# Kernel optimization log

Measured on AMD Instinct MI355X. Metric: run time of the kernel, lower is better.

The kernel has to match this reference:

```python
import jax, jax.numpy as jnp
import numpy as np

B, NH, M, XD = 8192, 128, 4096, 1024
ALPHA_1, SIGMA_1 = 100.0, 0.02
MAX_ITER = 30  # FastBarrierProjectionNoUpper(max_iter=30)


def cayley(W):
    """Cayley orthogonalization of a (possibly rectangular) matrix (out, in)."""
    cout, cin = W.shape
    if cout < cin:
        return cayley(W.T).T
    U, V = W[:cin], W[cin:]                 # U: (cin,cin), V: (cout-cin,cin)
    I = jnp.eye(cin, dtype=W.dtype)
    A = U - U.T + V.T @ V                   # skew + Gram
    iIpA = jnp.linalg.inv(I + A)
    return jnp.concatenate([iIpA @ (I - A), -2.0 * V @ iIpA], axis=0)


def cayley_linear(x, W, b, alpha):
    Q = cayley(alpha * W / jnp.linalg.norm(W))
    return x @ Q.T + b


def project_no_upper(lower, f_tilde):
    """Projection of f_tilde onto {f : sum(f)=0, f >= lower} per row.
    f*(lam) = max(f_tilde - lam, lower); Newton on g(lam)=sum f*(lam)=0,
    iterated a fixed MAX_ITER times (matches the 30-iter barrier solver)."""
    lam0 = jnp.mean(f_tilde, axis=-1, keepdims=True)

    def step(lam, _):
        f = jnp.maximum(f_tilde - lam, lower)
        g = jnp.sum(f, axis=-1, keepdims=True)
        active = jnp.sum((f_tilde - lam > lower).astype(f.dtype), axis=-1, keepdims=True)
        dg = -jnp.maximum(active, 1.0)      # g'(lam), safeguarded
        return lam - g / dg, None

    lam, _ = jax.lax.scan(step, lam0, None, length=MAX_ITER)
    return jnp.maximum(f_tilde - lam, lower)


def setup_inputs() -> dict:
    key = jax.random.key(0)
    ks = jax.random.split(key, 8)
    h = jax.random.uniform(ks[0], (B, NH), dtype=jnp.float32)
    h = h / jnp.sum(h, axis=-1, keepdims=True)      # state lives on the simplex
    x = jax.random.normal(ks[1], (B, XD), dtype=jnp.float32)

    def mk_w(k, shape):
        return jax.random.normal(k, shape, dtype=jnp.float32) * 0.05

    W_hm = mk_w(ks[2], (M, NH))
    W_mm = mk_w(ks[3], (M, M))
    W_mh = mk_w(ks[4], (NH, M))
    W_ux = mk_w(ks[5], (M, XD))
    b_hm = jnp.zeros((M,), jnp.float32)
    b_mm = jnp.zeros((M,), jnp.float32)
    b_mh = jnp.zeros((NH,), jnp.float32)
    b_ux = jnp.zeros((M,), jnp.float32)
    # CayleyLinear alpha initialized to ||W||_F (so alpha*W/||W|| == W at init)
    a_hm = jnp.linalg.norm(W_hm)
    a_mm = jnp.linalg.norm(W_mm)
    a_mh = jnp.linalg.norm(W_mh)
    a_ux = jnp.linalg.norm(W_ux)
    return {"h": h, "x": x,
            "W_hm": W_hm, "b_hm": b_hm, "a_hm": a_hm,
            "W_mm": W_mm, "b_mm": b_mm, "a_mm": a_mm,
            "W_mh": W_mh, "b_mh": b_mh, "a_mh": a_mh,
            "W_ux": W_ux, "b_ux": b_ux, "a_ux": a_ux}


def reference(h, x, W_hm, b_hm, a_hm, W_mm, b_mm, a_mm,
              W_mh, b_mh, a_mh, W_ux, b_ux, a_ux):
    # _h_dot_raw (dropout identity in eval mode)
    z = cayley_linear(h, W_hm, b_hm, a_hm) + cayley_linear(x, W_ux, b_ux, a_ux)
    z = jax.nn.relu(z)
    z = jax.nn.relu(cayley_linear(z, W_mm, b_mm, a_mm))
    f_tilde = cayley_linear(z, W_mh, b_mh, a_mh)   # [B, NH]
    # barrier lower bound keeping h >= 0 forward-invariant
    lower = -ALPHA_1 * (jnp.exp(SIGMA_1 * h) - 1.0)
    return project_no_upper(lower, f_tilde)
```

## Files before the change

kernel.cpp:

```cpp
#include <hip/hip_runtime.h>
#include <math.h>

#define ALPHA_1 100.0f
#define SIGMA_1 0.02f

typedef unsigned short bf16_t;
typedef short  bf16x8  __attribute__((ext_vector_type(8)));
typedef float  floatx4 __attribute__((ext_vector_type(4)));

typedef __attribute__((address_space(1))) void glb_void;
typedef __attribute__((address_space(3))) void lds_void;

__device__ __forceinline__ float bf2f(bf16_t u){ return __uint_as_float(((unsigned)u)<<16); }
__device__ __forceinline__ bf16_t f2bf(float f){
  unsigned u = __float_as_uint(f);
  u += 0x7FFFu + ((u>>16)&1u);
  return (bf16_t)(u>>16);
}

__device__ __forceinline__ void split4(float4 v, ushort4& h, ushort4& l){
  h.x=f2bf(v.x); h.y=f2bf(v.y); h.z=f2bf(v.z); h.w=f2bf(v.w);
  l.x=f2bf(v.x-bf2f(h.x)); l.y=f2bf(v.y-bf2f(h.y));
  l.z=f2bf(v.z-bf2f(h.z)); l.w=f2bf(v.w-bf2f(h.w));
}

__device__ __forceinline__ float4 load4f(const float* p){ return *(const float4*)p; }
__device__ __forceinline__ float loadS(const float* p){ return *p; }
__device__ __forceinline__ float loadS(const bf16_t* p){ return bf2f(*p); }
__device__ __forceinline__ void storeS(float* p, float v){ *p = v; }
__device__ __forceinline__ void storeS(bf16_t* p, float v){ *p = f2bf(v); }

__device__ __forceinline__ void async_copy16(void* lds, const void* g){
  __builtin_amdgcn_global_load_lds((glb_void*)g, (lds_void*)lds, 16, 0, 0);
}

template<typename TC, int RELU>
__global__ __launch_bounds__(256) void mfma_nt_kernel(
    int Mm, int Nn, int Kk,
    const bf16_t* __restrict__ A, int lda,
    const bf16_t* __restrict__ B, int ldb,
    TC* __restrict__ C, int ldc,
    const float* __restrict__ bias)
{
  __shared__ bf16_t As[128*64];
  __shared__ bf16_t Bs[128*64];
  const int tid  = threadIdx.x;
  const int lane = tid & 63, wv = tid >> 6;
  const int m0 = (int)(blockIdx.y << 7), n0 = (int)(blockIdx.x << 7);
  const int wm = (wv >> 1) << 6, wn = (wv & 1) << 6;
  const int rbase = wv << 5;

  floatx4 acc[4][4] = {};

  for (int kk = 0; kk < Kk; kk += 64){
    __syncthreads();
#pragma unroll
    for (int q=0;q<4;q++){
      int row = rbase + (q<<3) + (lane>>3);
      int cg  = (lane&7) ^ (row&7);
      async_copy16(&As[(size_t)(rbase+(q<<3))<<6],
                   A + (size_t)(m0+row)*lda + kk + (cg<<3));
      async_copy16(&Bs[(size_t)(rbase+(q<<3))<<6],
                   B + (size_t)(n0+row)*ldb + kk + (cg<<3));
    }
    __syncthreads();
#pragma unroll
    for (int ks=0; ks<2; ks++){
      bf16x8 af[4], bf[4];
      int quad = lane>>4, mr = lane&15;
      int c = quad + (ks<<2);
#pragma unroll
      for (int i=0;i<4;i++){
        int rowa = wm + i*16 + mr;
        af[i] = *(const bf16x8*)&As[(rowa<<6) + ((c ^ (rowa&7))<<3)];
        int rowb = wn + i*16 + mr;
        bf[i] = *(const bf16x8*)&Bs[(rowb<<6) + ((c ^ (rowb&7))<<3)];
      }
#pragma unroll
      for (int i=0;i<4;i++)
#pragma unroll
        for (int j=0;j<4;j++)
          acc[i][j] = __builtin_amdgcn_mfma_f32_16x16x32_bf16(af[i], bf[j], acc[i][j], 0,0,0);
    }
  }
#pragma unroll
  for (int i=0;i<4;i++){
#pragma unroll
    for (int j=0;j<4;j++){
      int rbase2 = m0 + wm + i*16 + (lane>>4)*4;
      int col    = n0 + wn + j*16 + (lane&15);
      float bv = bias ? bias[col] : 0.0f;
#pragma unroll
      for (int r=0;r<4;r++){
        float v = acc[i][j][r] + bv;
        if (RELU) v = fmaxf(v, 0.0f);
        storeS(&C[(size_t)(rbase2+r)*ldc + col], v);
      }
    }
  }
}

template<typename TC>
__global__ __launch_bounds__(256) void fgemm_nt_kernel(
    int Mm, int Nn, int Kk,
    const float* __restrict__ A, int lda,
    const float* __restrict__ Bt, int ldb,
    TC* __restrict__ C, int ldc,
    float alpha, const float* __restrict__ alpha_ptr, float beta, int skipk)
{
  __shared__ bf16_t Ah[128*64], Al[128*64], Bh[128*64], Bl[128*64];
  const int tid = threadIdx.x;
  const int lane = tid & 63, wv = tid >> 6;
  int by = blockIdx.y; if (by >= skipk) by++;
  const int m0 = by << 7, n0 = blockIdx.x << 7;
  const int wm = (wv >> 1) << 6, wn = (wv & 1) << 6;
  floatx4 acc[4][4] = {};

  for (int kk = 0; kk < Kk; kk += 64){
    float4 va[8], vb[8];
#pragma unroll
    for (int i=0;i<8;i++){
      int idx = (tid<<3) + i;
      int row = idx >> 4;
      int cg  = idx & 15;
      va[i] = load4f(A  + (size_t)(m0+row)*lda + kk + (cg<<2));
      vb[i] = load4f(Bt + (size_t)(n0+row)*ldb + kk + (cg<<2));
    }
    __syncthreads();
#pragma unroll
    for (int i=0;i<8;i++){
      int idx = (tid<<3) + i;
      int row = idx >> 4, cg = idx & 15;
      int off = (row<<6) + (((cg>>1) ^ (row&7))<<3) + ((cg&1)<<2);
      ushort4 hv, lv; split4(va[i], hv, lv);
      *(ushort4*)&Ah[off] = hv; *(ushort4*)&Al[off] = lv;
      ushort4 hw, lw; split4(vb[i], hw, lw);
      *(ushort4*)&Bh[off] = hw; *(ushort4*)&Bl[off] = lw;
    }
    __syncthreads();
#pragma unroll
    for (int ks=0; ks<2; ks++){
      int quad = lane>>4, mr = lane&15;
      int c = quad + (ks<<2);
      bf16x8 ah[4], al[4], bh[4], bl[4];
#pragma unroll
      for (int i=0;i<4;i++){
        int rowa = wm + i*16 + mr; int sa = (rowa<<6) + ((c ^ (rowa&7))<<3);
        ah[i] = *(const bf16x8*)&Ah[sa]; al[i] = *(const bf16x8*)&Al[sa];
        int rowb = wn + i*16 + mr; int sb = (rowb<<6) + ((c ^ (rowb&7))<<3);
        bh[i] = *(const bf16x8*)&Bh[sb]; bl[i] = *(const bf16x8*)&Bl[sb];
      }
#pragma unroll
      for (int i=0;i<4;i++)
#pragma unroll
        for (int j=0;j<4;j++){
          acc[i][j] = __builtin_amdgcn_mfma_f32_16x16x32_bf16(ah[i], bl[j], acc[i][j], 0,0,0);
          acc[i][j] = __builtin_amdgcn_mfma_f32_16x16x32_bf16(al[i], bh[j], acc[i][j], 0,0,0);
          acc[i][j] = __builtin_amdgcn_mfma_f32_16x16x32_bf16(ah[i], bh[j], acc[i][j], 0,0,0);
        }
    }
    __syncthreads();
  }
  float am = alpha;
  if (alpha_ptr) am *= *alpha_ptr;
#pragma unroll
  for (int i=0;i<4;i++){
#pragma unroll
    for (int j=0;j<4;j++){
      int rb = m0 + wm + i*16 + (lane>>4)*4;
      int col = n0 + wn + j*16 + (lane&15);
#pragma unroll
      for (int r=0;r<4;r++){
        size_t off = (size_t)(rb+r)*ldc + col;
        float v = am * acc[i][j][r];
        if (beta != 0.0f) v = fmaf(beta, loadS(&C[off]), v);
        storeS(&C[off], v);
      }
    }
  }
}

__global__ __launch_bounds__(1024) void invert128_kernel(
    const float* __restrict__ src, int ld,
    float* __restrict__ dst, float* __restrict__ dstT)
{
  __shared__ float brow[2][8*36];
  const int t = threadIdx.x;
  const int r = t>>3, sub = t&7;
  const int lane = t & 63;
  const int cb = (sub&3)<<5;
  const bool isA = sub < 4;
  float own[32];
  if (isA){
#pragma unroll
    for (int i=0;i<32;i++) own[i] = src[(size_t)r*ld + cb + i];
  } else {
#pragma unroll
    for (int i=0;i<32;i++) own[i] = (cb+i == r) ? 1.0f : 0.0f;
  }
  for (int pb=0; pb<4; pb++){
#pragma unroll
    for (int pi=0; pi<32; pi++){
      const int p = (pb<<5) + pi;
      float f = __shfl(own[pi], (lane & 56) | pb);
      float* bw = brow[p & 1];
      if (r == p){
        float ip = 1.0f / f;
#pragma unroll
        for (int i=0;i<32;i++) own[i] *= ip;
#pragma unroll
        for (int i=0;i<8;i++){
          float4 v;
          v.x = own[(i<<2)+0]; v.y = own[(i<<2)+1];
          v.z = own[(i<<2)+2]; v.w = own[(i<<2)+3];
          *(float4*)&bw[sub*36 + (i<<2)] = v;
        }
      }
      __syncthreads();
      if (r != p){
#pragma unroll
        for (int i=0;i<8;i++){
          float4 b = *(const float4*)&bw[sub*36 + (i<<2)];
          own[(i<<2)+0] = fmaf(-f, b.x, own[(i<<2)+0]);
          own[(i<<2)+1] = fmaf(-f, b.y, own[(i<<2)+1]);
          own[(i<<2)+2] = fmaf(-f, b.z, own[(i<<2)+2]);
          own[(i<<2)+3] = fmaf(-f, b.w, own[(i<<2)+3]);
        }
      }
    }
  }
  if (!isA){
#pragma unroll
    for (int i=0;i<32;i++){
      dst [(size_t)r*128 + cb + i] = own[i];
      dstT[(size_t)(cb+i)*128 + r] = own[i];
    }
  }
}


__device__ void tile_to_lds(
    const float* __restrict__ Min, int n, int k, int r, int c,
    const bf16_t* __restrict__ Gh, const bf16_t* __restrict__ Gl,
    const bf16_t* __restrict__ Th, const bf16_t* __restrict__ Tl,
    float* __restrict__ Dst, char* __restrict__ stage, int tid)
{
  if (c == k){
    const bf16_t* sh = Gh + ((size_t)r<<14);
    const bf16_t* sl = Gl + ((size_t)r<<14);
    for (int q=tid; q<4096; q+=1024){
      int rr=q>>5, c4=(q&31)<<2;
      ushort4 hv=*(const ushort4*)&sh[(rr<<7)+c4];
      ushort4 lv=*(const ushort4*)&sl[(rr<<7)+c4];
      Dst[rr*132+c4+0]=bf2f(hv.x)+bf2f(lv.x);
      Dst[rr*132+c4+1]=bf2f(hv.y)+bf2f(lv.y);
      Dst[rr*132+c4+2]=bf2f(hv.z)+bf2f(lv.z);
      Dst[rr*132+c4+3]=bf2f(hv.w)+bf2f(lv.w);
    }
    __syncthreads();
    return;
  }
  bf16_t* Ah=(bf16_t*)stage;           bf16_t* Al=(bf16_t*)(stage+16384);
  bf16_t* Bh=(bf16_t*)(stage+32768);   bf16_t* Bl=(bf16_t*)(stage+49152);
  const int lane = tid & 63, wv = tid >> 6;
  const int wm = (wv >> 2) << 5, wn = (wv & 3) << 5;
  const bf16_t* gh = Gh + ((size_t)r<<14);
  const bf16_t* gl = Gl + ((size_t)r<<14);
  const bf16_t* th = Th + ((size_t)c<<14);
  const bf16_t* tl = Tl + ((size_t)c<<14);
  floatx4 acc[2][2] = {};
#pragma unroll
  for (int kk = 0; kk < 128; kk += 64){
    __syncthreads();
#pragma unroll
    for (int s=0;s<2;s++){
      int idx = tid + (s<<10);
      int row = idx >> 4, cg = idx & 15;
      int off = (row<<6) + (((cg>>1) ^ (row&7))<<3) + ((cg&1)<<2);
      *(ushort4*)&Ah[off] = *(const ushort4*)&gh[(row<<7) + kk + (cg<<2)];
      *(ushort4*)&Al[off] = *(const ushort4*)&gl[(row<<7) + kk + (cg<<2)];
      *(ushort4*)&Bh[off] = *(const ushort4*)&th[(row<<7) + kk + (cg<<2)];
      *(ushort4*)&Bl[off] = *(const ushort4*)&tl[(row<<7) + kk + (cg<<2)];
    }
    __syncthreads();
#pragma unroll
    for (int ks=0; ks<2; ks++){
      int quad = lane>>4, mr = lane&15;
      int cc = quad + (ks<<2);
      bf16x8 ah[2], al[2], bh[2], bl[2];
#pragma unroll
      for (int i=0;i<2;i++){
        int rowa = wm + i*16 + mr; int sa = (rowa<<6) + ((cc ^ (rowa&7))<<3);
        ah[i] = *(const bf16x8*)&Ah[sa]; al[i] = *(const bf16x8*)&Al[sa];
        int rowb = wn + i*16 + mr; int sb = (rowb<<6) + ((cc ^ (rowb&7))<<3);
        bh[i] = *(const bf16x8*)&Bh[sb]; bl[i] = *(const bf16x8*)&Bl[sb];
      }
#pragma unroll
      for (int i=0;i<2;i++)
#pragma unroll
        for (int j=0;j<2;j++){
          acc[i][j] = __builtin_amdgcn_mfma_f32_16x16x32_bf16(ah[i], bl[j], acc[i][j], 0,0,0);
          acc[i][j] = __builtin_amdgcn_mfma_f32_16x16x32_bf16(al[i], bh[j], acc[i][j], 0,0,0);
          acc[i][j] = __builtin_amdgcn_mfma_f32_16x16x32_bf16(ah[i], bh[j], acc[i][j], 0,0,0);
        }
    }
  }
  const int addin = (r != k);
#pragma unroll
  for (int i=0;i<2;i++)
#pragma unroll
    for (int j=0;j<2;j++){
      int rb = wm + i*16 + ((lane>>4)<<2);
      int col = wn + j*16 + (lane&15);
#pragma unroll
      for (int r4=0;r4<4;r4++){
        float v = acc[i][j][r4];
        if (addin) v += Min[(size_t)((r<<7)+rb+r4)*n + (c<<7) + col];
        Dst[(rb+r4)*132 + col] = v;
      }
    }
  __syncthreads();
}

__device__ void prep1024(
    const float* __restrict__ Mc, int n, int k, int ib,
    bf16_t* __restrict__ Gh, bf16_t* __restrict__ Gl,
    bf16_t* __restrict__ Th, bf16_t* __restrict__ Tl,
    char* smraw, int t)
{
  float* browB = (float*)smraw;
  float* Pl    = (float*)(smraw + 2304);
  float* Ast   = (float*)(smraw + 69888);
  const int r = t>>3, sub = t&7;
  const int lane = t & 63;
  const int cb = (sub&3)<<5;
  const bool isA = sub < 4;
  const float* D = Mc + ((size_t)(k<<7))*n + (k<<7);
  float own[32];
  if (isA){
#pragma unroll
    for (int q=0;q<32;q++) own[q] = D[(size_t)r*n + cb + q];
  } else {
#pragma unroll
    for (int q=0;q<32;q++) own[q] = (cb+q == r) ? 1.0f : 0.0f;
  }
  for (int pb=0; pb<4; pb++){
#pragma unroll
    for (int pi=0; pi<32; pi++){
      const int p = (pb<<5) + pi;
      float f = __shfl(own[pi], (lane & 56) | pb);
      float* bw = browB + (p & 1)*288;
      if (r == p){
        float ip = 1.0f / f;
#pragma unroll
        for (int q=0;q<32;q++) own[q] *= ip;
#pragma unroll
        for (int q=0;q<8;q++){
          float4 v;
          v.x=own[(q<<2)+0]; v.y=own[(q<<2)+1]; v.z=own[(q<<2)+2]; v.w=own[(q<<2)+3];
          *(float4*)&bw[sub*36 + (q<<2)] = v;
        }
      }
      __syncthreads();
      if (r != p){
#pragma unroll
        for (int q=0;q<8;q++){
          float4 b = *(const float4*)&bw[sub*36 + (q<<2)];
          own[(q<<2)+0] = fmaf(-f, b.x, own[(q<<2)+0]);
          own[(q<<2)+1] = fmaf(-f, b.y, own[(q<<2)+1]);
          own[(q<<2)+2] = fmaf(-f, b.z, own[(q<<2)+2]);
          own[(q<<2)+3] = fmaf(-f, b.w, own[(q<<2)+3]);
        }
      }
    }
  }
  if (!isA){
#pragma unroll
    for (int q=0;q<8;q++){
      float4 v;
      v.x=own[(q<<2)+0]; v.y=own[(q<<2)+1]; v.z=own[(q<<2)+2]; v.w=own[(q<<2)+3];
      *(float4*)&Pl[r*132 + cb + (q<<2)] = v;
      if (ib == k){
        ushort4 hv, lv; split4(v, hv, lv);
        *(ushort4*)&Gh[((size_t)k<<14) + (r<<7) + cb + (q<<2)] = hv;
        *(ushort4*)&Gl[((size_t)k<<14) + (r<<7) + cb + (q<<2)] = lv;
      }
    }
  }
  __syncthreads();
  if (ib == k) return;

  const float* Ski = Mc + ((size_t)(k<<7))*n + (ib<<7);
#pragma unroll
  for (int q=0;q<4;q++){
    int f4 = (t<<2) + q;
    int rr = f4>>5, c4 = (f4&31)<<2;
    *(float4*)&Ast[rr*132 + c4] = *(const float4*)&Ski[(size_t)rr*n + c4];
  }
  __syncthreads();
#pragma unroll
  for (int q=0;q<4;q++){
    int f4 = (t<<2) + q;
    int cc = f4>>5, r4 = (f4&31)<<2;
    float4 v;
    v.x = Ast[(r4+0)*132 + cc]; v.y = Ast[(r4+1)*132 + cc];
    v.z = Ast[(r4+2)*132 + cc]; v.w = Ast[(r4+3)*132 + cc];
    ushort4 hv, lv; split4(v, hv, lv);
    *(ushort4*)&Th[((size_t)ib<<14) + (cc<<7) + r4] = hv;
    *(ushort4*)&Tl[((size_t)ib<<14) + (cc<<7) + r4] = lv;
  }
  __syncthreads();

  const float* Sik = Mc + ((size_t)(ib<<7))*n + (k<<7);
#pragma unroll
  for (int q=0;q<4;q++){
    int f4 = (t<<2) + q;
    int rr = f4>>5, c4 = (f4&31)<<2;
    *(float4*)&Ast[rr*132 + c4] = *(const float4*)&Sik[(size_t)rr*n + c4];
  }
  __syncthreads();

  const int tx = t&31, ty = t>>5;
  const int r0 = ty<<2, c0 = tx<<2;
  float acc[4][4] = {};
  for (int kq=0; kq<128; kq++){
    float4 b = *(const float4*)&Pl[kq*132 + c0];
    float a0 = Ast[(r0+0)*132 + kq];
    float a1 = Ast[(r0+1)*132 + kq];
    float a2 = Ast[(r0+2)*132 + kq];
    float a3 = Ast[(r0+3)*132 + kq];
    acc[0][0]=fmaf(a0,b.x,acc[0][0]); acc[0][1]=fmaf(a0,b.y,acc[0][1]);
    acc[0][2]=fmaf(a0,b.z,acc[0][2]); acc[0][3]=fmaf(a0,b.w,acc[0][3]);
    acc[1][0]=fmaf(a1,b.x,acc[1][0]); acc[1][1]=fmaf(a1,b.y,acc[1][1]);
    acc[1][2]=fmaf(a1,b.z,acc[1][2]); acc[1][3]=fmaf(a1,b.w,acc[1][3]);
    acc[2][0]=fmaf(a2,b.x,acc[2][0]); acc[2][1]=fmaf(a2,b.y,acc[2][1]);
    acc[2][2]=fmaf(a2,b.z,acc[2][2]); acc[2][3]=fmaf(a2,b.w,acc[2][3]);
    acc[3][0]=fmaf(a3,b.x,acc[3][0]); acc[3][1]=fmaf(a3,b.y,acc[3][1]);
    acc[3][2]=fmaf(a3,b.z,acc[3][2]); acc[3][3]=fmaf(a3,b.w,acc[3][3]);
  }
#pragma unroll
  for (int rr=0;rr<4;rr++){
    float4 v; v.x=-acc[rr][0]; v.y=-acc[rr][1]; v.z=-acc[rr][2]; v.w=-acc[rr][3];
    ushort4 hv, lv; split4(v, hv, lv);
    *(ushort4*)&Gh[((size_t)ib<<14) + ((size_t)(r0+rr)<<7) + c0] = hv;
    *(ushort4*)&Gl[((size_t)ib<<14) + ((size_t)(r0+rr)<<7) + c0] = lv;
  }
}

__device__ void prep_fused(
    const float* __restrict__ Min, int n, int k, int ib,
    const bf16_t* __restrict__ Gh, const bf16_t* __restrict__ Gl,
    const bf16_t* __restrict__ Th, const bf16_t* __restrict__ Tl,
    bf16_t* __restrict__ Gnh, bf16_t* __restrict__ Gnl,
    bf16_t* __restrict__ Tnh, bf16_t* __restrict__ Tnl,
    char* smraw, int t)
{
  const int kp = k+1;
  float* browB = (float*)smraw;
  float* Pl    = (float*)(smraw + 2304);
  float* Ast   = (float*)(smraw + 69888);
  char*  stage = (char*)(smraw + 2304);

  tile_to_lds(Min, n, k, kp, kp, Gh, Gl, Th, Tl, Ast, stage, t);

  const int r = t>>3, sub = t&7;
  const int lane = t & 63;
  const int cb = (sub&3)<<5;
  const bool isA = sub < 4;
  float own[32];
  if (isA){
#pragma unroll
    for (int q=0;q<8;q++)
      *(float4*)&own[q<<2] = *(const float4*)&Ast[r*132 + cb + (q<<2)];
  } else {
#pragma unroll
    for (int q=0;q<32;q++) own[q] = (cb+q == r) ? 1.0f : 0.0f;
  }
  __syncthreads();
  for (int pb=0; pb<4; pb++){
#pragma unroll
    for (int pi=0; pi<32; pi++){
      const int p = (pb<<5) + pi;
      float f = __shfl(own[pi], (lane & 56) | pb);
      float* bw = browB + (p & 1)*288;
      if (r == p){
        float ip = 1.0f / f;
#pragma unroll
        for (int q=0;q<32;q++) own[q] *= ip;
#pragma unroll
        for (int q=0;q<8;q++){
          float4 v;
          v.x=own[(q<<2)+0]; v.y=own[(q<<2)+1]; v.z=own[(q<<2)+2]; v.w=own[(q<<2)+3];
          *(float4*)&bw[sub*36 + (q<<2)] = v;
        }
      }
      __syncthreads();
      if (r != p){
#pragma unroll
        for (int q=0;q<8;q++){
          float4 b = *(const float4*)&bw[sub*36 + (q<<2)];
          own[(q<<2)+0] = fmaf(-f, b.x, own[(q<<2)+0]);
          own[(q<<2)+1] = fmaf(-f, b.y, own[(q<<2)+1]);
          own[(q<<2)+2] = fmaf(-f, b.z, own[(q<<2)+2]);
          own[(q<<2)+3] = fmaf(-f, b.w, own[(q<<2)+3]);
        }
      }
    }
  }
  if (ib == kp){
    if (!isA){
#pragma unroll
      for (int q=0;q<8;q++){
        float4 v;
        v.x=own[(q<<2)+0]; v.y=own[(q<<2)+1]; v.z=own[(q<<2)+2]; v.w=own[(q<<2)+3];
        ushort4 hv, lv; split4(v, hv, lv);
        *(ushort4*)&Gnh[((size_t)kp<<14) + (r<<7) + cb + (q<<2)] = hv;
        *(ushort4*)&Gnl[((size_t)kp<<14) + (r<<7) + cb + (q<<2)] = lv;
      }
    }
    return;
  }

  tile_to_lds(Min, n, k, kp, ib, Gh, Gl, Th, Tl, Ast, stage, t);
#pragma unroll
  for (int q=0;q<4;q++){
    int f4 = (t<<2) + q;
    int cc = f4>>5, r4 = (f4&31)<<2;
    float4 v;
    v.x = Ast[(r4+0)*132 + cc]; v.y = Ast[(r4+1)*132 + cc];
    v.z = Ast[(r4+2)*132 + cc]; v.w = Ast[(r4+3)*132 + cc];
    ushort4 hv, lv; split4(v, hv, lv);
    *(ushort4*)&Tnh[((size_t)ib<<14) + (cc<<7) + r4] = hv;
    *(ushort4*)&Tnl[((size_t)ib<<14) + (cc<<7) + r4] = lv;
  }
  __syncthreads();

  tile_to_lds(Min, n, k, ib, kp, Gh, Gl, Th, Tl, Ast, stage, t);

  if (!isA){
#pragma unroll
    for (int q=0;q<8;q++){
      float4 v;
      v.x=own[(q<<2)+0]; v.y=own[(q<<2)+1]; v.z=own[(q<<2)+2]; v.w=own[(q<<2)+3];
      *(float4*)&Pl[r*132 + cb + (q<<2)] = v;
    }
  }
  __syncthreads();

  const int tx = t&31, ty = t>>5;
  const int r0 = ty<<2, c0 = tx<<2;
  float acc[4][4] = {};
  for (int kq=0; kq<128; kq++){
    float4 b = *(const float4*)&Pl[kq*132 + c0];
    float a0 = Ast[(r0+0)*132 + kq];
    float a1 = Ast[(r0+1)*132 + kq];
    float a2 = Ast[(r0+2)*132 + kq];
    float a3 = Ast[(r0+3)*132 + kq];
    acc[0][0]=fmaf(a0,b.x,acc[0][0]); acc[0][1]=fmaf(a0,b.y,acc[0][1]);
    acc[0][2]=fmaf(a0,b.z,acc[0][2]); acc[0][3]=fmaf(a0,b.w,acc[0][3]);
    acc[1][0]=fmaf(a1,b.x,acc[1][0]); acc[1][1]=fmaf(a1,b.y,acc[1][1]);
    acc[1][2]=fmaf(a1,b.z,acc[1][2]); acc[1][3]=fmaf(a1,b.w,acc[1][3]);
    acc[2][0]=fmaf(a2,b.x,acc[2][0]); acc[2][1]=fmaf(a2,b.y,acc[2][1]);
    acc[2][2]=fmaf(a2,b.z,acc[2][2]); acc[2][3]=fmaf(a2,b.w,acc[2][3]);
    acc[3][0]=fmaf(a3,b.x,acc[3][0]); acc[3][1]=fmaf(a3,b.y,acc[3][1]);
    acc[3][2]=fmaf(a3,b.z,acc[3][2]); acc[3][3]=fmaf(a3,b.w,acc[3][3]);
  }
#pragma unroll
  for (int rr=0;rr<4;rr++){
    float4 v; v.x=-acc[rr][0]; v.y=-acc[rr][1]; v.z=-acc[rr][2]; v.w=-acc[rr][3];
    ushort4 hv, lv; split4(v, hv, lv);
    *(ushort4*)&Gnh[((size_t)ib<<14) + ((size_t)(r0+rr)<<7) + c0] = hv;
    *(ushort4*)&Gnl[((size_t)ib<<14) + ((size_t)(r0+rr)<<7) + c0] = lv;
  }
}

__device__ void update_tile1024(
    const float* __restrict__ Min, float* __restrict__ Mout, int n, int k,
    int by, int bx,
    const bf16_t* __restrict__ Gh, const bf16_t* __restrict__ Gl,
    const bf16_t* __restrict__ Th, const bf16_t* __restrict__ Tl,
    char* sm, int tid)
{
  if (bx == k){
    const bf16_t* sh = Gh + ((size_t)by<<14);
    const bf16_t* sl = Gl + ((size_t)by<<14);
    float* dst = Mout + ((size_t)(by<<7))*n + ((size_t)k<<7);
    for (int q=tid; q<4096; q+=1024){
      int r=q>>5, c4=(q&31)<<2;
      ushort4 hv=*(const ushort4*)&sh[(r<<7)+c4];
      ushort4 lv=*(const ushort4*)&sl[(r<<7)+c4];
      float4 v; v.x=bf2f(hv.x)+bf2f(lv.x); v.y=bf2f(hv.y)+bf2f(lv.y);
                v.z=bf2f(hv.z)+bf2f(lv.z); v.w=bf2f(hv.w)+bf2f(lv.w);
      *(float4*)&dst[(size_t)r*n + c4] = v;
    }
    return;
  }
  bf16_t* Ah=(bf16_t*)sm;           bf16_t* Al=(bf16_t*)(sm+16384);
  bf16_t* Bh=(bf16_t*)(sm+32768);   bf16_t* Bl=(bf16_t*)(sm+49152);
  const int lane = tid & 63, wv = tid >> 6;
  const int wm = (wv >> 2) << 5, wn = (wv & 3) << 5;
  const bf16_t* gh = Gh + ((size_t)by<<14);
  const bf16_t* gl = Gl + ((size_t)by<<14);
  const bf16_t* th = Th + ((size_t)bx<<14);
  const bf16_t* tl = Tl + ((size_t)bx<<14);
  floatx4 acc[2][2] = {};

#pragma unroll
  for (int kk = 0; kk < 128; kk += 64){
    __syncthreads();
#pragma unroll
    for (int s=0;s<2;s++){
      int idx = tid + (s<<10);
      int row = idx >> 4, cg = idx & 15;
      int off = (row<<6) + (((cg>>1) ^ (row&7))<<3) + ((cg&1)<<2);
      *(ushort4*)&Ah[off] = *(const ushort4*)&gh[(row<<7) + kk + (cg<<2)];
      *(ushort4*)&Al[off] = *(const ushort4*)&gl[(row<<7) + kk + (cg<<2)];
      *(ushort4*)&Bh[off] = *(const ushort4*)&th[(row<<7) + kk + (cg<<2)];
      *(ushort4*)&Bl[off] = *(const ushort4*)&tl[(row<<7) + kk + (cg<<2)];
    }
    __syncthreads();
#pragma unroll
    for (int ks=0; ks<2; ks++){
      int quad = lane>>4, mr = lane&15;
      int c = quad + (ks<<2);
      bf16x8 ah[2], al[2], bh[2], bl[2];
#pragma unroll
      for (int i=0;i<2;i++){
        int rowa = wm + i*16 + mr; int sa = (rowa<<6) + ((c ^ (rowa&7))<<3);
        ah[i] = *(const bf16x8*)&Ah[sa]; al[i] = *(const bf16x8*)&Al[sa];
        int rowb = wn + i*16 + mr; int sb = (rowb<<6) + ((c ^ (rowb&7))<<3);
        bh[i] = *(const bf16x8*)&Bh[sb]; bl[i] = *(const bf16x8*)&Bl[sb];
      }
#pragma unroll
      for (int i=0;i<2;i++)
#pragma unroll
        for (int j=0;j<2;j++){
          acc[i][j] = __builtin_amdgcn_mfma_f32_16x16x32_bf16(ah[i], bl[j], acc[i][j], 0,0,0);
          acc[i][j] = __builtin_amdgcn_mfma_f32_16x16x32_bf16(al[i], bh[j], acc[i][j], 0,0,0);
          acc[i][j] = __builtin_amdgcn_mfma_f32_16x16x32_bf16(ah[i], bh[j], acc[i][j], 0,0,0);
        }
    }
  }
  const int addin = (by != k);
#pragma unroll
  for (int i=0;i<2;i++)
#pragma unroll
    for (int j=0;j<2;j++){
      int rb = (by<<7) + wm + i*16 + ((lane>>4)<<2);
      int col = (bx<<7) + wn + j*16 + (lane&15);
#pragma unroll
      for (int r4=0;r4<4;r4++){
        size_t off = (size_t)(rb+r4)*n + col;
        float v = acc[i][j][r4];
        if (addin) v += Min[off];
        Mout[off] = v;
      }
    }
}

__global__ __launch_bounds__(1024) void gj_prep0_kernel(
    const float* __restrict__ M, int n,
    bf16_t* Gh, bf16_t* Gl, bf16_t* Th, bf16_t* Tl)
{
  __shared__ char sm[137472] __attribute__((aligned(16)));
  prep1024(M, n, 0, blockIdx.x, Gh, Gl, Th, Tl, sm, threadIdx.x);
}

__global__ __launch_bounds__(1024) void gj_stepF_kernel(
    const float* __restrict__ Min, float* __restrict__ Mout, int n, int k,
    const bf16_t* __restrict__ Gh, const bf16_t* __restrict__ Gl,
    const bf16_t* __restrict__ Th, const bf16_t* __restrict__ Tl,
    bf16_t* Gnh, bf16_t* Gnl, bf16_t* Tnh, bf16_t* Tnl)
{
  __shared__ char sm[137472] __attribute__((aligned(16)));
  const int nb = n >> 7;
  const int bid = blockIdx.x, tid = threadIdx.x;
  if (bid < nb){
    prep_fused(Min, n, k, bid, Gh, Gl, Th, Tl, Gnh, Gnl, Tnh, Tnl, sm, tid);
  } else {
    int q = bid - nb;
    int by = q / nb, bx = q - by*nb;
    update_tile1024(Min, Mout, n, k, by, bx, Gh, Gl, Th, Tl, sm, tid);
  }
}

__global__ __launch_bounds__(1024) void gj_stepL_kernel(
    const float* __restrict__ Min, float* __restrict__ Mout, int n, int k,
    const bf16_t* __restrict__ Gh, const bf16_t* __restrict__ Gl,
    const bf16_t* __restrict__ Th, const bf16_t* __restrict__ Tl)
{
  __shared__ char sm[65536] __attribute__((aligned(16)));
  const int nb = n >> 7;
  int by = blockIdx.x / nb, bx = blockIdx.x - by*nb;
  update_tile1024(Min, Mout, n, k, by, bx, Gh, Gl, Th, Tl, sm, threadIdx.x);
}

template<int TRANS>
__global__ __launch_bounds__(256) void gram_partial_kernel(
    const float* __restrict__ V, int ldv, int n, int Ks,
    float* __restrict__ Gp)
{
  __shared__ float Vi[16][132];
  __shared__ float Vj[16][132];
  const int cj = blockIdx.x, ci = blockIdx.y, z = blockIdx.z;
  const int tid = threadIdx.x;
  const int i0 = ci<<7, j0 = cj<<7;
  const int tx = tid&15, ty = tid>>4;
  float acc[8][8] = {};
  for (int k0 = z*Ks; k0 < (z+1)*Ks; k0 += 16){
    if (TRANS == 0){
      for (int q=tid; q<512; q+=256){
        int kr = q>>5, c4 = (q&31)<<2;
        *(float4*)&Vi[kr][c4] = *(const float4*)&V[(size_t)(k0+kr)*ldv + i0 + c4];
        *(float4*)&Vj[kr][c4] = *(const float4*)&V[(size_t)(k0+kr)*ldv + j0 + c4];
      }
    } else {
      for (int q=tid; q<512; q+=256){
        int c = q>>2, qq = (q&3)<<2;
        float4 a = *(const float4*)&V[(size_t)(i0+c)*ldv + k0 + qq];
        Vi[qq+0][c]=a.x; Vi[qq+1][c]=a.y; Vi[qq+2][c]=a.z; Vi[qq+3][c]=a.w;
        float4 b = *(const float4*)&V[(size_t)(j0+c)*ldv + k0 + qq];
        Vj[qq+0][c]=b.x; Vj[qq+1][c]=b.y; Vj[qq+2][c]=b.z; Vj[qq+3][c]=b.w;
      }
    }
    __syncthreads();
#pragma unroll
    for (int kr=0; kr<16; kr++){
      float a[8], b[8];
      *(float4*)&a[0] = *(const float4*)&Vi[kr][(ty<<3)];
      *(float4*)&a[4] = *(const float4*)&Vi[kr][(ty<<3)+4];
      *(float4*)&b[0] = *(const float4*)&Vj[kr][(tx<<3)];
      *(float4*)&b[4] = *(const float4*)&Vj[kr][(tx<<3)+4];
#pragma unroll
      for (int i=0;i<8;i++)
#pragma unroll
        for (int jj=0;jj<8;jj++) acc[i][jj] = fmaf(a[i], b[jj], acc[i][jj]);
    }
    __syncthreads();
  }
#pragma unroll
  for (int i=0;i<8;i++)
#pragma unroll
    for (int jj=0;jj<8;jj++)
      Gp[(size_t)z*n*n + (size_t)(i0+(ty<<3)+i)*n + j0+(tx<<3)+jj] = acc[i][jj];
}

__global__ void sumsq_kernel(const float* __restrict__ w, int n, float* __restrict__ acc){
  float s = 0.0f;
  for (int i = blockIdx.x*blockDim.x + threadIdx.x; i < n; i += gridDim.x*blockDim.x){
    float v = w[i]; s = fmaf(v, v, s);
  }
#pragma unroll
  for (int o=32;o;o>>=1) s += __shfl_xor(s, o);
  if ((threadIdx.x & 63) == 0) atomicAdd(acc, s);
}

__global__ void scales_kernel(float* scal, const float* a0, const float* a1,
                              const float* a2, const float* a3){
  if (threadIdx.x==0 && blockIdx.x==0){
    float s;
    s = a0[0]/sqrtf(scal[0]); scal[4]=s; scal[8]=s*s;
    s = a1[0]/sqrtf(scal[1]); scal[5]=s; scal[9]=s*s;
    s = a2[0]/sqrtf(scal[2]); scal[6]=s; scal[10]=s*s;
    s = a3[0]/sqrtf(scal[3]); scal[7]=s; scal[11]=s*s;
  }
}

__global__ void build_mm_kernel(const float* __restrict__ W, const float* __restrict__ scal,
                                float* __restrict__ Mo){
  int j = (blockIdx.x<<4) + (threadIdx.x&15);
  int i = (blockIdx.y<<4) + (threadIdx.x>>4);
  float s = scal[5];
  float a = s*(W[((size_t)i<<12)+j] - W[((size_t)j<<12)+i]);
  Mo[((size_t)i<<12)+j] = ((i==j)?1.0f:0.0f) + a;
}

__global__ void build_rect_kernel(const float* __restrict__ W, int ldw, int transw, int n,
      const float* __restrict__ Gp, int S,
      const float* __restrict__ scal, int sidx, int sidx2,
      float* __restrict__ Mo){
  int j = (blockIdx.x<<4)+(threadIdx.x&15);
  int i = (blockIdx.y<<4)+(threadIdx.x>>4);
  float s = scal[sidx], s2 = scal[sidx2];
  float wij = transw ? W[(size_t)j*ldw+i] : W[(size_t)i*ldw+j];
  float wji = transw ? W[(size_t)i*ldw+j] : W[(size_t)j*ldw+i];
  float g = 0.0f;
  for (int ss=0; ss<S; ss++) g += Gp[(size_t)ss*n*n + (size_t)i*n + j];
  Mo[(size_t)i*n + j] = ((i==j)?1.0f:0.0f) + s*(wij - wji) + s2*g;
}

template<typename TD>
__global__ void qtop_kernel(const float* __restrict__ X, int n,
                            TD* __restrict__ dst, int ldd){
  int j = blockIdx.x*blockDim.x + threadIdx.x;
  int i = blockIdx.y;
  if (j<n) storeS(&dst[(size_t)i*ldd+j],
                  2.0f*X[(size_t)i*n+j] - ((i==j)?1.0f:0.0f));
}

__global__ void transposeF_kernel(const float* __restrict__ src, int ls,
                                  float* __restrict__ dst, int ld){
  __shared__ float t[32][33];
  int c0 = blockIdx.x<<5, r0 = blockIdx.y<<5;
  int tx = threadIdx.x & 31, ty = threadIdx.x >> 5;
#pragma unroll
  for (int i=0;i<4;i++) t[ty+i*8][tx] = src[(size_t)(r0+ty+i*8)*ls + c0+tx];
  __syncthreads();
#pragma unroll
  for (int i=0;i<4;i++) dst[(size_t)(c0+ty+i*8)*ld + r0+tx] = t[tx][ty+i*8];
}

__global__ void pack_A_kernel(const float* __restrict__ h, const float* __restrict__ x,
                              bf16_t* __restrict__ Ap){
  int c = blockIdx.x*blockDim.x + threadIdx.x;
  int m = blockIdx.y;
  if (c >= 2176) return;
  float v;
  if (c < 128)       v = h[(size_t)m*128 + c];
  else if (c < 1152) v = x[(size_t)m*1024 + (c-128)];
  else {
    float xv = x[(size_t)m*1024 + (c-1152)];
    v = xv - bf2f(f2bf(xv));
  }
  Ap[(size_t)m*2176 + c] = f2bf(v);
}

__global__ void dup_kernel(bf16_t* __restrict__ Bp){
  int c = blockIdx.x*blockDim.x + threadIdx.x;
  int r = blockIdx.y;
  Bp[(size_t)r*2176 + 1152 + c] = Bp[(size_t)r*2176 + 128 + c];
}

__global__ void addvec_kernel(const float* __restrict__ a, const float* __restrict__ b,
                              float* __restrict__ c, int n){
  int i = blockIdx.x*blockDim.x + threadIdx.x;
  if (i<n) c[i] = a[i] + b[i];
}

__global__ __launch_bounds__(256) void project_kernel(
    const float* __restrict__ ft, const float* __restrict__ h, float* __restrict__ out){
  int row  = (blockIdx.x<<2) + (threadIdx.x>>6);
  int lane = threadIdx.x & 63;
  const float* fr = ft + ((size_t)row<<7);
  const float* hr = h  + ((size_t)row<<7);
  float f0 = fr[lane], f1 = fr[lane+64];
  float l0 = -ALPHA_1*(expf(SIGMA_1*hr[lane])   - 1.0f);
  float l1 = -ALPHA_1*(expf(SIGMA_1*hr[lane+64])- 1.0f);
  float s = f0 + f1;
#pragma unroll
  for (int o=32;o;o>>=1) s += __shfl_xor(s, o);
  float lam = s * (1.0f/128.0f);
  for (int it=0; it<30; it++){
    float a0 = f0 - lam, a1 = f1 - lam;
    float g = fmaxf(a0,l0) + fmaxf(a1,l1);
    float c = (a0>l0 ? 1.0f:0.0f) + (a1>l1 ? 1.0f:0.0f);
#pragma unroll
    for (int o=32;o;o>>=1){ g += __shfl_xor(g,o); c += __shfl_xor(c,o); }
    lam += g / fmaxf(c, 1.0f);
  }
  out[((size_t)row<<7)+lane]    = fmaxf(f0-lam, l0);
  out[((size_t)row<<7)+lane+64] = fmaxf(f1-lam, l1);
}

template<typename TC, int RELU>
static inline void mfma_nt(hipStream_t st, int Mm, int Nn, int Kk,
    const bf16_t* A, int lda, const bf16_t* B, int ldb, TC* C, int ldc,
    const float* bias){
  dim3 grid(Nn>>7, Mm>>7);
  mfma_nt_kernel<TC,RELU><<<grid, 256, 0, st>>>(Mm,Nn,Kk,A,lda,B,ldb,C,ldc,bias);
}

template<typename TC>
static inline void fgemm(hipStream_t st, int Mm, int Nn, int Kk,
    const float* A, int lda, const float* Bt, int ldb, TC* C, int ldc,
    float alpha, const float* aptr, float beta){
  dim3 grid(Nn>>7, Mm>>7);
  fgemm_nt_kernel<TC><<<grid, 256, 0, st>>>(Mm,Nn,Kk,A,lda,Bt,ldb,C,ldc,
                                            alpha,aptr,beta, 1<<30);
}

static void gj_inverse5(hipStream_t st, float* M, float* Mtmp, int n,
    bf16_t* Gh, bf16_t* Gl, bf16_t* Th, bf16_t* Tl){
  const int nb = n >> 7;
  const size_t gstep = (size_t)nb << 14;
  gj_prep0_kernel<<<nb, 1024, 0, st>>>(M, n, Gh, Gl, Th, Tl);
  for (int k=0; k<nb; k++){
    const float* Min = (k&1) ? Mtmp : M;
    float* Mout      = (k&1) ? M : Mtmp;
    const size_t pc = (size_t)(k&1)*gstep, pn = (size_t)((k&1)^1)*gstep;
    if (k < nb-1){
      gj_stepF_kernel<<<nb + nb*nb, 1024, 0, st>>>(Min, Mout, n, k,
          Gh+pc, Gl+pc, Th+pc, Tl+pc,
          Gh+pn, Gl+pn, Th+pn, Tl+pn);
    } else {
      gj_stepL_kernel<<<nb*nb, 1024, 0, st>>>(Min, Mout, n, k,
          Gh+pc, Gl+pc, Th+pc, Tl+pc);
    }
  }
}

extern "C" void kernel_launch(void* const* d_in, const int* in_sizes, int n_in,
                              void* d_out, int out_size, void* d_ws, size_t ws_size,
                              hipStream_t stream){
  (void)in_sizes; (void)n_in; (void)out_size; (void)ws_size;
  const float* h    = (const float*)d_in[0];
  const float* x    = (const float*)d_in[1];
  const float* Whm  = (const float*)d_in[2];
  const float* bhm  = (const float*)d_in[3];
  const float* ahm  = (const float*)d_in[4];
  const float* Wmm  = (const float*)d_in[5];
  const float* bmm  = (const float*)d_in[6];
  const float* amm  = (const float*)d_in[7];
  const float* Wmh  = (const float*)d_in[8];
  const float* bmh  = (const float*)d_in[9];
  const float* amh  = (const float*)d_in[10];
  const float* Wux  = (const float*)d_in[11];
  const float* bux  = (const float*)d_in[12];
  const float* auxs = (const float*)d_in[13];
  float* out = (float*)d_out;

  char* wp = (char*)d_ws;
  auto alloc = [&](size_t bytes)->void*{
    void* p = (void*)wp; wp += (bytes + 255) & ~(size_t)255; return p; };
  float*  scal   = (float*)alloc(4096);
  float*  Mhm    = (float*)alloc((size_t)128*128*4);
  float*  Mmh    = (float*)alloc((size_t)128*128*4);
  float*  P128   = (float*)alloc((size_t)128*128*4);
  float*  PT128  = (float*)alloc((size_t)128*128*4);
  bf16_t* GhB    = (bf16_t*)alloc((size_t)2*32*16384*2);
  bf16_t* GlB    = (bf16_t*)alloc((size_t)2*32*16384*2);
  bf16_t* ThB    = (bf16_t*)alloc((size_t)2*32*16384*2);
  bf16_t* TlB    = (bf16_t*)alloc((size_t)2*32*16384*2);
  bf16_t* Qmh_b  = (bf16_t*)alloc((size_t)128*4096*2);
  float*  bsum   = (float*)alloc((size_t)4096*4);
  bf16_t* Bp     = (bf16_t*)alloc((size_t)4096*2176*2);
  float*  R1     = (float*)alloc((size_t)4096*4096*4);
  float*  R2     = (float*)alloc((size_t)4096*4096*4);
  bf16_t* Qmmb   = (bf16_t*)alloc((size_t)4096*4096*2);
  float*  gram23 = R1;
  float*  WmhTv  = R1 + (size_t)1024*1024;
  float*  Mmm  = R1;
  bf16_t* Ap   = (bf16_t*)R1;
  bf16_t* z2   = (bf16_t*)R1;
  float*  Mux  = R2 + (size_t)1024*1024;
  float*  XuxT = R2 + (size_t)5*1024*1024;
  float*  Gp1  = R2 + (size_t)6*1024*1024;
  bf16_t* z    = (bf16_t*)R2;
  float*  ftl  = R2;

  hipMemsetAsync(scal, 0, 16*sizeof(float), stream);
  sumsq_kernel<<<512,256,0,stream>>>(Whm, 4096*128,  scal+0);
  sumsq_kernel<<<512,256,0,stream>>>(Wmm, 4096*4096, scal+1);
  sumsq_kernel<<<512,256,0,stream>>>(Wmh, 128*4096,  scal+2);
  sumsq_kernel<<<512,256,0,stream>>>(Wux, 4096*1024, scal+3);
  scales_kernel<<<1,1,0,stream>>>(scal, ahm, amm, amh, auxs);

  gram_partial_kernel<0><<<dim3(8,8,4),256,0,stream>>>(
      Wux + (size_t)1024*1024, 1024, 1024, 768, Gp1);
  build_rect_kernel<<<dim3(64,64),256,0,stream>>>(Wux,1024,0,1024, Gp1,4, scal,7,11, Mux);
  gj_inverse5(stream, Mux, R1, 1024, GhB, GlB, ThB, TlB);
  transposeF_kernel<<<dim3(32,32),256,0,stream>>>(Mux, 1024, XuxT, 1024);
  qtop_kernel<bf16_t><<<dim3(4,1024),256,0,stream>>>(Mux, 1024, Bp+128, 2176);
  fgemm<bf16_t>(stream, 3072,1024,1024, Wux+(size_t)1024*1024,1024, XuxT,1024,
                Bp+(size_t)1024*2176+128, 2176, -2.0f,&scal[7], 0.0f);

  gram_partial_kernel<0><<<dim3(1,1,31),256,0,stream>>>(
      Whm + (size_t)128*128, 128, 128, 128, gram23);
  build_rect_kernel<<<dim3(8,8),256,0,stream>>>(Whm,128,0,128, gram23,31, scal,4,8, Mhm);
  invert128_kernel<<<1,1024,0,stream>>>(Mhm,128,P128,PT128);
  qtop_kernel<bf16_t><<<dim3(1,128),256,0,stream>>>(P128, 128, Bp, 2176);
  fgemm<bf16_t>(stream, 3968,128,128, Whm+128*128,128, PT128,128,
                Bp+(size_t)128*2176, 2176, -2.0f,&scal[4], 0.0f);

  gram_partial_kernel<1><<<dim3(1,1,31),256,0,stream>>>(
      Wmh + 128, 4096, 128, 128, gram23);
  build_rect_kernel<<<dim3(8,8),256,0,stream>>>(Wmh,4096,1,128, gram23,31, scal,6,10, Mmh);
  invert128_kernel<<<1,1024,0,stream>>>(Mmh,128,P128,PT128);
  qtop_kernel<bf16_t><<<dim3(1,128),256,0,stream>>>(PT128, 128, Qmh_b, 4096);
  transposeF_kernel<<<dim3(124,4),256,0,stream>>>(Wmh+128, 4096, WmhTv, 128);
  fgemm<bf16_t>(stream, 128,3968,128, PT128,128, WmhTv,128,
                Qmh_b+128, 4096, -2.0f,&scal[6], 0.0f);

  build_mm_kernel<<<dim3(256,256),256,0,stream>>>(Wmm, scal, Mmm);
  gj_inverse5(stream, Mmm, R2, 4096, GhB, GlB, ThB, TlB);
  qtop_kernel<bf16_t><<<dim3(16,4096),256,0,stream>>>(Mmm, 4096, Qmmb, 4096);

  pack_A_kernel<<<dim3(9,8192),256,0,stream>>>(h, x, Ap);
  dup_kernel<<<dim3(4,4096),256,0,stream>>>(Bp);
  addvec_kernel<<<16,256,0,stream>>>(bhm, bux, bsum, 4096);

  mfma_nt<bf16_t,1>(stream, 8192,4096,2176, Ap,2176, Bp,2176, z,4096, bsum);
  mfma_nt<bf16_t,1>(stream, 8192,4096,4096, z,4096, Qmmb,4096, z2,4096, bmm);
  mfma_nt<float,0>(stream, 8192, 128,4096, z2,4096, Qmh_b,4096, ftl,128, bmh);

  project_kernel<<<2048,256,0,stream>>>(ftl, h, out);
}
```

Measured before the change: 5.112 ms.

## Shrink fused Gauss-Jordan step LDS footprint by chunking pivot panel and unpadded tiles

```diff
diff --git a/kernel.cpp b/kernel.cpp
--- a/kernel.cpp
+++ b/kernel.cpp
@@ -252,10 +252,10 @@
       int rr=q>>5, c4=(q&31)<<2;
       ushort4 hv=*(const ushort4*)&sh[(rr<<7)+c4];
       ushort4 lv=*(const ushort4*)&sl[(rr<<7)+c4];
-      Dst[rr*132+c4+0]=bf2f(hv.x)+bf2f(lv.x);
-      Dst[rr*132+c4+1]=bf2f(hv.y)+bf2f(lv.y);
-      Dst[rr*132+c4+2]=bf2f(hv.z)+bf2f(lv.z);
-      Dst[rr*132+c4+3]=bf2f(hv.w)+bf2f(lv.w);
+      Dst[(rr<<7)+c4+0]=bf2f(hv.x)+bf2f(lv.x);
+      Dst[(rr<<7)+c4+1]=bf2f(hv.y)+bf2f(lv.y);
+      Dst[(rr<<7)+c4+2]=bf2f(hv.z)+bf2f(lv.z);
+      Dst[(rr<<7)+c4+3]=bf2f(hv.w)+bf2f(lv.w);
     }
     __syncthreads();
     return;
@@ -305,6 +305,7 @@
         }
     }
   }
+  __syncthreads();
   const int addin = (r != k);
 #pragma unroll
   for (int i=0;i<2;i++)
@@ -316,7 +317,7 @@
       for (int r4=0;r4<4;r4++){
         float v = acc[i][j][r4];
         if (addin) v += Min[(size_t)((r<<7)+rb+r4)*n + (c<<7) + col];
-        Dst[(rb+r4)*132 + col] = v;
+        Dst[((rb+r4)<<7) + col] = v;
       }
     }
   __syncthreads();
@@ -456,10 +457,10 @@
     char* smraw, int t)
 {
   const int kp = k+1;
-  float* browB = (float*)smraw;
-  float* Pl    = (float*)(smraw + 2304);
-  float* Ast   = (float*)(smraw + 69888);
-  char*  stage = (char*)(smraw + 2304);
+  float* Ast   = (float*)smraw;
+  char*  stage = smraw;
+  float* Pbuf  = (float*)(smraw + 65536);
+  float* browB = (float*)(smraw + 65536);
 
   tile_to_lds(Min, n, k, kp, kp, Gh, Gl, Th, Tl, Ast, stage, t);
 
@@ -471,7 +472,7 @@
   if (isA){
 #pragma unroll
     for (int q=0;q<8;q++)
-      *(float4*)&own[q<<2] = *(const float4*)&Ast[r*132 + cb + (q<<2)];
+      *(float4*)&own[q<<2] = *(const float4*)&Ast[(r<<7) + cb + (q<<2)];
   } else {
 #pragma unroll
     for (int q=0;q<32;q++) own[q] = (cb+q == r) ? 1.0f : 0.0f;
@@ -527,8 +528,8 @@
     int f4 = (t<<2) + q;
     int cc = f4>>5, r4 = (f4&31)<<2;
     float4 v;
-    v.x = Ast[(r4+0)*132 + cc]; v.y = Ast[(r4+1)*132 + cc];
-    v.z = Ast[(r4+2)*132 + cc]; v.w = Ast[(r4+3)*132 + cc];
+    v.x = Ast[((r4+0)<<7) + cc]; v.y = Ast[((r4+1)<<7) + cc];
+    v.z = Ast[((r4+2)<<7) + cc]; v.w = Ast[((r4+3)<<7) + cc];
     ushort4 hv, lv; split4(v, hv, lv);
     *(ushort4*)&Tnh[((size_t)ib<<14) + (cc<<7) + r4] = hv;
     *(ushort4*)&Tnl[((size_t)ib<<14) + (cc<<7) + r4] = lv;
@@ -537,33 +538,38 @@
 
   tile_to_lds(Min, n, k, ib, kp, Gh, Gl, Th, Tl, Ast, stage, t);
 
-  if (!isA){
-#pragma unroll
-    for (int q=0;q<8;q++){
-      float4 v;
-      v.x=own[(q<<2)+0]; v.y=own[(q<<2)+1]; v.z=own[(q<<2)+2]; v.w=own[(q<<2)+3];
-      *(float4*)&Pl[r*132 + cb + (q<<2)] = v;
-    }
-  }
-  __syncthreads();
-
   const int tx = t&31, ty = t>>5;
   const int r0 = ty<<2, c0 = tx<<2;
   float acc[4][4] = {};
-  for (int kq=0; kq<128; kq++){
-    float4 b = *(const float4*)&Pl[kq*132 + c0];
-    float a0 = Ast[(r0+0)*132 + kq];
-    float a1 = Ast[(r0+1)*132 + kq];
-    float a2 = Ast[(r0+2)*132 + kq];
-    float a3 = Ast[(r0+3)*132 + kq];
-    acc[0][0]=fmaf(a0,b.x,acc[0][0]); acc[0][1]=fmaf(a0,b.y,acc[0][1]);
-    acc[0][2]=fmaf(a0,b.z,acc[0][2]); acc[0][3]=fmaf(a0,b.w,acc[0][3]);
-    acc[1][0]=fmaf(a1,b.x,acc[1][0]); acc[1][1]=fmaf(a1,b.y,acc[1][1]);
-    acc[1][2]=fmaf(a1,b.z,acc[1][2]); acc[1][3]=fmaf(a1,b.w,acc[1][3]);
-    acc[2][0]=fmaf(a2,b.x,acc[2][0]); acc[2][1]=fmaf(a2,b.y,acc[2][1]);
-    acc[2][2]=fmaf(a2,b.z,acc[2][2]); acc[2][3]=fmaf(a2,b.w,acc[2][3]);
-    acc[3][0]=fmaf(a3,b.x,acc[3][0]); acc[3][1]=fmaf(a3,b.y,acc[3][1]);
-    acc[3][2]=fmaf(a3,b.z,acc[3][2]); acc[3][3]=fmaf(a3,b.w,acc[3][3]);
+  for (int kc=0; kc<4; kc++){
+    const int kk = kc<<5;
+    if (!isA && r >= kk && r < kk+32){
+#pragma unroll
+      for (int q=0;q<8;q++){
+        float4 v;
+        v.x=own[(q<<2)+0]; v.y=own[(q<<2)+1]; v.z=own[(q<<2)+2]; v.w=own[(q<<2)+3];
+        *(float4*)&Pbuf[((r-kk)<<7) + cb + (q<<2)] = v;
+      }
+    }
+    __syncthreads();
+#pragma unroll
+    for (int kq2=0; kq2<32; kq2++){
+      const int kq = kk + kq2;
+      float4 b = *(const float4*)&Pbuf[(kq2<<7) + c0];
+      float a0 = Ast[((r0+0)<<7) + kq];
+      float a1 = Ast[((r0+1)<<7) + kq];
+      float a2 = Ast[((r0+2)<<7) + kq];
+      float a3 = Ast[((r0+3)<<7) + kq];
+      acc[0][0]=fmaf(a0,b.x,acc[0][0]); acc[0][1]=fmaf(a0,b.y,acc[0][1]);
+      acc[0][2]=fmaf(a0,b.z,acc[0][2]); acc[0][3]=fmaf(a0,b.w,acc[0][3]);
+      acc[1][0]=fmaf(a1,b.x,acc[1][0]); acc[1][1]=fmaf(a1,b.y,acc[1][1]);
+      acc[1][2]=fmaf(a1,b.z,acc[1][2]); acc[1][3]=fmaf(a1,b.w,acc[1][3]);
+      acc[2][0]=fmaf(a2,b.x,acc[2][0]); acc[2][1]=fmaf(a2,b.y,acc[2][1]);
+      acc[2][2]=fmaf(a2,b.z,acc[2][2]); acc[2][3]=fmaf(a2,b.w,acc[2][3]);
+      acc[3][0]=fmaf(a3,b.x,acc[3][0]); acc[3][1]=fmaf(a3,b.y,acc[3][1]);
+      acc[3][2]=fmaf(a3,b.z,acc[3][2]); acc[3][3]=fmaf(a3,b.w,acc[3][3]);
+    }
+    __syncthreads();
   }
 #pragma unroll
   for (int rr=0;rr<4;rr++){
@@ -672,7 +678,7 @@
     const bf16_t* __restrict__ Th, const bf16_t* __restrict__ Tl,
     bf16_t* Gnh, bf16_t* Gnl, bf16_t* Tnh, bf16_t* Tnl)
 {
-  __shared__ char sm[137472] __attribute__((aligned(16)));
+  __shared__ char sm[81920] __attribute__((aligned(16)));
   const int nb = n >> 7;
   const int bid = blockIdx.x, tid = threadIdx.x;
   if (bid < nb){
```

After: 5.443 ms. 6.5% more time.
